# Optimization experiments

Hardware: AMD Instinct MI355X
Metric: run time of the kernel (lower is better)

## Reference

```python
import jax, jax.numpy as jnp
import numpy as np

N_CLUSTERS = 512
FEAT_DIM = 256
ALPHA = 1.0


def setup_inputs() -> dict:
    key = jax.random.key(0)
    kx, kc = jax.random.split(key)
    x = jax.random.normal(kx, (262144, FEAT_DIM), dtype=jnp.float32)
    # xavier_normal for [n_clusters, feat_dim]: std = sqrt(2/(fan_in+fan_out))
    std = float(np.sqrt(2.0 / (N_CLUSTERS + FEAT_DIM)))
    clusters = jax.random.normal(kc, (N_CLUSTERS, FEAT_DIM), dtype=jnp.float32) * std
    return {"x": x, "clusters": clusters}


def reference(x, clusters):
    x_sq = jnp.sum(x * x, axis=1, keepdims=True)            # [N, 1]
    c_sq = jnp.sum(clusters * clusters, axis=1)[None, :]     # [1, K]
    cross = jnp.einsum('nd,kd->nk', x, clusters)             # [N, K]
    dist2 = jnp.maximum(x_sq + c_sq - 2.0 * cross, 0.0) / ALPHA
    q = 1.0 / (1.0 + dist2)
    q = q ** ((ALPHA + 1.0) / 2.0)
    return q / jnp.sum(q, axis=1, keepdims=True)
```

## Files before the change

### kernel.cpp

```cpp
#include <hip/hip_runtime.h>
#include <cstdint>
#include <cstddef>

#define N_ROWS  262144
#define FEAT    256
#define NCLUST  512

#define BM      64
#define THREADS 512

typedef __attribute__((ext_vector_type(8))) __bf16 bf16x8;
typedef __attribute__((ext_vector_type(4))) float  floatx4;

__device__ __forceinline__ unsigned short f2bf(float f) {
    union { float f; unsigned u; } v; v.f = f;
    unsigned u = v.u;
    u += 0x7FFFu + ((u >> 16) & 1u);
    return (unsigned short)(u >> 16);
}

__global__ __launch_bounds__(64) void prep_kernel(const float* __restrict__ clusters,
                                                  unsigned short* __restrict__ cb,
                                                  float* __restrict__ csq) {
    const int row = blockIdx.x;
    const int t   = threadIdx.x;
    const float4* src = (const float4*)(clusters + (size_t)row * FEAT);
    float4 v = src[t];
    float ss = v.x*v.x + v.y*v.y + v.z*v.z + v.w*v.w;
    ushort4 o;
    o.x = f2bf(v.x); o.y = f2bf(v.y); o.z = f2bf(v.z); o.w = f2bf(v.w);

    const int ntile = row >> 4;
    const int l16   = row & 15;
    const int kk    = t >> 3;
    const int quad  = (t >> 1) & 3;
    const int half  = t & 1;
    const size_t g  = (size_t)((ntile * 8 + kk) * 64 + quad * 16 + l16);
    *(ushort4*)(cb + g * 8 + half * 4) = o;

    #pragma unroll
    for (int m = 32; m > 0; m >>= 1) ss += __shfl_xor(ss, m);
    if (t == 0) csq[row] = ss;
}

__global__ __launch_bounds__(THREADS, 4) void cluster_kernel(
    const float* __restrict__ x,
    const unsigned short* __restrict__ cb,
    const float* __restrict__ csq,
    float* __restrict__ out)
{
    __shared__ unsigned short As[BM][FEAT + 8];
    __shared__ float s_xsq[BM];
    __shared__ float s_rpart[8][BM];
    __shared__ float s_rinv[BM];

    const int tid  = threadIdx.x;
    const int row0 = blockIdx.x * BM;

    {
        const int r = tid >> 3;
        const int j = tid & 7;
        const float4* xg = (const float4*)(x + (size_t)(row0 + r) * FEAT);
        float ss = 0.f;
        #pragma unroll
        for (int i = 0; i < 8; i++) {
            float4 v = xg[j + 8 * i];
            ss += v.x*v.x + v.y*v.y + v.z*v.z + v.w*v.w;
            ushort4 o;
            o.x = f2bf(v.x); o.y = f2bf(v.y); o.z = f2bf(v.z); o.w = f2bf(v.w);
            *(ushort4*)&As[r][(j + 8 * i) * 4] = o;
        }
        ss += __shfl_xor(ss, 1);
        ss += __shfl_xor(ss, 2);
        ss += __shfl_xor(ss, 4);
        if (j == 0) s_xsq[r] = ss;
    }
    __syncthreads();

    const int wave = tid >> 6;
    const int lane = tid & 63;
    const int quad = lane >> 4;
    const int l16  = lane & 15;

    floatx4 acc[4][4];
    #pragma unroll
    for (int mt = 0; mt < 4; mt++)
        #pragma unroll
        for (int nt = 0; nt < 4; nt++)
            acc[mt][nt] = (floatx4){0.f, 0.f, 0.f, 0.f};

    const unsigned short* bq[4];
    #pragma unroll
    for (int nt = 0; nt < 4; nt++)
        bq[nt] = cb + ((size_t)((wave * 4 + nt) * 8) * 64 + lane) * 8;

    #pragma unroll 2
    for (int s = 0; s < 8; s++) {
        bf16x8 a[4], b[4];
        #pragma unroll
        for (int mt = 0; mt < 4; mt++)
            a[mt] = *(const bf16x8*)&As[mt * 16 + l16][s * 32 + quad * 8];
        #pragma unroll
        for (int nt = 0; nt < 4; nt++)
            b[nt] = *(const bf16x8*)(bq[nt] + (size_t)s * 512);
        #pragma unroll
        for (int mt = 0; mt < 4; mt++)
            #pragma unroll
            for (int nt = 0; nt < 4; nt++)
                acc[mt][nt] = __builtin_amdgcn_mfma_f32_16x16x32_bf16(
                    a[mt], b[nt], acc[mt][nt], 0, 0, 0);
    }

    float csqv[4];
    #pragma unroll
    for (int nt = 0; nt < 4; nt++)
        csqv[nt] = csq[wave * 64 + nt * 16 + l16];

    #pragma unroll
    for (int mt = 0; mt < 4; mt++) {
        #pragma unroll
        for (int r = 0; r < 4; r++) {
            const int m = mt * 16 + quad * 4 + r;
            float xs = s_xsq[m];
            float rp = 0.f;
            #pragma unroll
            for (int nt = 0; nt < 4; nt++) {
                float d2 = xs + csqv[nt] - 2.0f * acc[mt][nt][r];
                d2 = fmaxf(d2, 0.f);
                float q = __builtin_amdgcn_rcpf(1.0f + d2);
                acc[mt][nt][r] = q;
                rp += q;
            }
            rp += __shfl_xor(rp, 1);
            rp += __shfl_xor(rp, 2);
            rp += __shfl_xor(rp, 4);
            rp += __shfl_xor(rp, 8);
            if (l16 == 0) s_rpart[wave][m] = rp;
        }
    }
    __syncthreads();
    if (tid < BM) {
        float t = 0.f;
        #pragma unroll
        for (int w = 0; w < 8; w++) t += s_rpart[w][tid];
        s_rinv[tid] = __builtin_amdgcn_rcpf(t);
    }
    __syncthreads();

    float* op = out + (size_t)row0 * NCLUST + wave * 64 + l16;
    #pragma unroll
    for (int mt = 0; mt < 4; mt++) {
        #pragma unroll
        for (int r = 0; r < 4; r++) {
            const int m = mt * 16 + quad * 4 + r;
            const float inv = s_rinv[m];
            #pragma unroll
            for (int nt = 0; nt < 4; nt++)
                op[(size_t)m * NCLUST + nt * 16] = acc[mt][nt][r] * inv;
        }
    }
}

extern "C" void kernel_launch(void* const* d_in, const int* in_sizes, int n_in,
                              void* d_out, int out_size, void* d_ws, size_t ws_size,
                              hipStream_t stream) {
    const float* x        = (const float*)d_in[0];
    const float* clusters = (const float*)d_in[1];
    unsigned short* cb = (unsigned short*)d_ws;
    float* csq = (float*)((char*)d_ws + (size_t)NCLUST * FEAT * 2);
    float* out = (float*)d_out;

    prep_kernel<<<NCLUST, 64, 0, stream>>>(clusters, cb, csq);
    cluster_kernel<<<N_ROWS / BM, THREADS, 0, stream>>>(x, cb, csq, out);
}
```

Before: 751.2 us.

## Make cluster kernel persistent with double-buffered prefetch of next x tile

Launches a fixed grid of 512 blocks that each loop over several 64-row tiles, prefetching the next tile's x rows into registers during the MFMA and epilogue of the current tile and writing them into a second LDS buffer. The aim is to hide global load latency of x behind compute and output stores, and to amortize block launch and cluster-norm loads. It doubles LDS use and adds register pressure, which can lower occupancy and reduce the latency hiding that many independent blocks previously gave.

```diff
diff --git a/kernel.cpp b/kernel.cpp
--- a/kernel.cpp
+++ b/kernel.cpp
@@ -8,6 +8,9 @@
 
 #define BM      64
 #define THREADS 512
+#define NTILES  (N_ROWS / BM)
+#define GRID    512
+#define TPB     (NTILES / GRID)
 
 typedef __attribute__((ext_vector_type(8))) __bf16 bf16x8;
 typedef __attribute__((ext_vector_type(4))) float  floatx4;
@@ -49,114 +52,166 @@
     const float* __restrict__ csq,
     float* __restrict__ out)
 {
-    __shared__ unsigned short As[BM][FEAT + 8];
-    __shared__ float s_xsq[BM];
+    __shared__ unsigned short As[2][BM][FEAT + 8];
+    __shared__ float s_xsq[2][BM];
     __shared__ float s_rpart[8][BM];
     __shared__ float s_rinv[BM];
 
     const int tid  = threadIdx.x;
-    const int row0 = blockIdx.x * BM;
-
-    {
-        const int r = tid >> 3;
-        const int j = tid & 7;
-        const float4* xg = (const float4*)(x + (size_t)(row0 + r) * FEAT);
-        float ss = 0.f;
-        #pragma unroll
-        for (int i = 0; i < 8; i++) {
-            float4 v = xg[j + 8 * i];
-            ss += v.x*v.x + v.y*v.y + v.z*v.z + v.w*v.w;
-            ushort4 o;
-            o.x = f2bf(v.x); o.y = f2bf(v.y); o.z = f2bf(v.z); o.w = f2bf(v.w);
-            *(ushort4*)&As[r][(j + 8 * i) * 4] = o;
-        }
-        ss += __shfl_xor(ss, 1);
-        ss += __shfl_xor(ss, 2);
-        ss += __shfl_xor(ss, 4);
-        if (j == 0) s_xsq[r] = ss;
-    }
-    __syncthreads();
+    const int r    = tid >> 3;
+    const int j    = tid & 7;
 
     const int wave = tid >> 6;
     const int lane = tid & 63;
     const int quad = lane >> 4;
     const int l16  = lane & 15;
 
-    floatx4 acc[4][4];
-    #pragma unroll
-    for (int mt = 0; mt < 4; mt++)
-        #pragma unroll
-        for (int nt = 0; nt < 4; nt++)
-            acc[mt][nt] = (floatx4){0.f, 0.f, 0.f, 0.f};
+    const int tile0 = blockIdx.x * TPB;
 
     const unsigned short* bq[4];
     #pragma unroll
     for (int nt = 0; nt < 4; nt++)
         bq[nt] = cb + ((size_t)((wave * 4 + nt) * 8) * 64 + lane) * 8;
 
-    #pragma unroll 2
-    for (int s = 0; s < 8; s++) {
-        bf16x8 a[4], b[4];
-        #pragma unroll
-        for (int mt = 0; mt < 4; mt++)
-            a[mt] = *(const bf16x8*)&As[mt * 16 + l16][s * 32 + quad * 8];
-        #pragma unroll
-        for (int nt = 0; nt < 4; nt++)
-            b[nt] = *(const bf16x8*)(bq[nt] + (size_t)s * 512);
-        #pragma unroll
-        for (int mt = 0; mt < 4; mt++)
-            #pragma unroll
-            for (int nt = 0; nt < 4; nt++)
-                acc[mt][nt] = __builtin_amdgcn_mfma_f32_16x16x32_bf16(
-                    a[mt], b[nt], acc[mt][nt], 0, 0, 0);
-    }
-
     float csqv[4];
     #pragma unroll
     for (int nt = 0; nt < 4; nt++)
         csqv[nt] = csq[wave * 64 + nt * 16 + l16];
 
-    #pragma unroll
-    for (int mt = 0; mt < 4; mt++) {
-        #pragma unroll
-        for (int r = 0; r < 4; r++) {
-            const int m = mt * 16 + quad * 4 + r;
-            float xs = s_xsq[m];
-            float rp = 0.f;
-            #pragma unroll
-            for (int nt = 0; nt < 4; nt++) {
-                float d2 = xs + csqv[nt] - 2.0f * acc[mt][nt][r];
-                d2 = fmaxf(d2, 0.f);
-                float q = __builtin_amdgcn_rcpf(1.0f + d2);
-                acc[mt][nt][r] = q;
-                rp += q;
-            }
-            rp += __shfl_xor(rp, 1);
-            rp += __shfl_xor(rp, 2);
-            rp += __shfl_xor(rp, 4);
-            rp += __shfl_xor(rp, 8);
-            if (l16 == 0) s_rpart[wave][m] = rp;
-        }
+    float4 xa[4], xb[4];
+    {
+        const float4* xg = (const float4*)(x + (size_t)(tile0 * BM + r) * FEAT);
+        #pragma unroll
+        for (int i = 0; i < 4; i++) xa[i] = xg[j + 8 * i];
+        #pragma unroll
+        for (int i = 0; i < 4; i++) xb[i] = xg[j + 8 * i + 32];
+        float ss = 0.f;
+        #pragma unroll
+        for (int i = 0; i < 4; i++) {
+            float4 v = xa[i];
+            ss += v.x*v.x + v.y*v.y + v.z*v.z + v.w*v.w;
+            ushort4 o; o.x = f2bf(v.x); o.y = f2bf(v.y); o.z = f2bf(v.z); o.w = f2bf(v.w);
+            *(ushort4*)&As[0][r][(j + 8 * i) * 4] = o;
+        }
+        #pragma unroll
+        for (int i = 0; i < 4; i++) {
+            float4 v = xb[i];
+            ss += v.x*v.x + v.y*v.y + v.z*v.z + v.w*v.w;
+            ushort4 o; o.x = f2bf(v.x); o.y = f2bf(v.y); o.z = f2bf(v.z); o.w = f2bf(v.w);
+            *(ushort4*)&As[0][r][(j + 8 * i + 32) * 4] = o;
+        }
+        ss += __shfl_xor(ss, 1);
+        ss += __shfl_xor(ss, 2);
+        ss += __shfl_xor(ss, 4);
+        if (j == 0) s_xsq[0][r] = ss;
     }
     __syncthreads();
-    if (tid < BM) {
-        float t = 0.f;
-        #pragma unroll
-        for (int w = 0; w < 8; w++) t += s_rpart[w][tid];
-        s_rinv[tid] = __builtin_amdgcn_rcpf(t);
-    }
-    __syncthreads();
-
-    float* op = out + (size_t)row0 * NCLUST + wave * 64 + l16;
-    #pragma unroll
-    for (int mt = 0; mt < 4; mt++) {
-        #pragma unroll
-        for (int r = 0; r < 4; r++) {
-            const int m = mt * 16 + quad * 4 + r;
-            const float inv = s_rinv[m];
+
+    for (int it = 0; it < TPB; it++) {
+        const int  c       = it & 1;
+        const int  tile    = tile0 + it;
+        const bool hasnext = (it + 1 < TPB);
+        const float4* xg1  = (const float4*)(x + (size_t)((tile + 1) * BM + r) * FEAT);
+
+        if (hasnext) {
+            #pragma unroll
+            for (int i = 0; i < 4; i++) xa[i] = xg1[j + 8 * i];
+        }
+
+        floatx4 acc[4][4];
+        #pragma unroll
+        for (int mt = 0; mt < 4; mt++)
             #pragma unroll
             for (int nt = 0; nt < 4; nt++)
-                op[(size_t)m * NCLUST + nt * 16] = acc[mt][nt][r] * inv;
+                acc[mt][nt] = (floatx4){0.f, 0.f, 0.f, 0.f};
+
+        #pragma unroll 2
+        for (int s = 0; s < 8; s++) {
+            bf16x8 a[4], b[4];
+            #pragma unroll
+            for (int mt = 0; mt < 4; mt++)
+                a[mt] = *(const bf16x8*)&As[c][mt * 16 + l16][s * 32 + quad * 8];
+            #pragma unroll
+            for (int nt = 0; nt < 4; nt++)
+                b[nt] = *(const bf16x8*)(bq[nt] + (size_t)s * 512);
+            #pragma unroll
+            for (int mt = 0; mt < 4; mt++)
+                #pragma unroll
+                for (int nt = 0; nt < 4; nt++)
+                    acc[mt][nt] = __builtin_amdgcn_mfma_f32_16x16x32_bf16(
+                        a[mt], b[nt], acc[mt][nt], 0, 0, 0);
+        }
+
+        if (hasnext) {
+            #pragma unroll
+            for (int i = 0; i < 4; i++) xb[i] = xg1[j + 8 * i + 32];
+        }
+
+        #pragma unroll
+        for (int mt = 0; mt < 4; mt++) {
+            #pragma unroll
+            for (int rr = 0; rr < 4; rr++) {
+                const int m = mt * 16 + quad * 4 + rr;
+                float xs = s_xsq[c][m];
+                float rp = 0.f;
+                #pragma unroll
+                for (int nt = 0; nt < 4; nt++) {
+                    float d2 = xs + csqv[nt] - 2.0f * acc[mt][nt][rr];
+                    d2 = fmaxf(d2, 0.f);
+                    float q = __builtin_amdgcn_rcpf(1.0f + d2);
+                    acc[mt][nt][rr] = q;
+                    rp += q;
+                }
+                rp += __shfl_xor(rp, 1);
+                rp += __shfl_xor(rp, 2);
+                rp += __shfl_xor(rp, 4);
+                rp += __shfl_xor(rp, 8);
+                if (l16 == 0) s_rpart[wave][m] = rp;
+            }
+        }
+        __syncthreads();
+
+        if (tid < BM) {
+            float t = 0.f;
+            #pragma unroll
+            for (int w = 0; w < 8; w++) t += s_rpart[w][tid];
+            s_rinv[tid] = __builtin_amdgcn_rcpf(t);
+        }
+
+        if (hasnext) {
+            float ss = 0.f;
+            #pragma unroll
+            for (int i = 0; i < 4; i++) {
+                float4 v = xa[i];
+                ss += v.x*v.x + v.y*v.y + v.z*v.z + v.w*v.w;
+                ushort4 o; o.x = f2bf(v.x); o.y = f2bf(v.y); o.z = f2bf(v.z); o.w = f2bf(v.w);
+                *(ushort4*)&As[1 - c][r][(j + 8 * i) * 4] = o;
+            }
+            #pragma unroll
+            for (int i = 0; i < 4; i++) {
+                float4 v = xb[i];
+                ss += v.x*v.x + v.y*v.y + v.z*v.z + v.w*v.w;
+                ushort4 o; o.x = f2bf(v.x); o.y = f2bf(v.y); o.z = f2bf(v.z); o.w = f2bf(v.w);
+                *(ushort4*)&As[1 - c][r][(j + 8 * i + 32) * 4] = o;
+            }
+            ss += __shfl_xor(ss, 1);
+            ss += __shfl_xor(ss, 2);
+            ss += __shfl_xor(ss, 4);
+            if (j == 0) s_xsq[1 - c][r] = ss;
+        }
+        __syncthreads();
+
+        float* op = out + (size_t)(tile * BM) * NCLUST + wave * 64 + l16;
+        #pragma unroll
+        for (int mt = 0; mt < 4; mt++) {
+            #pragma unroll
+            for (int rr = 0; rr < 4; rr++) {
+                const int m = mt * 16 + quad * 4 + rr;
+                const float inv = s_rinv[m];
+                #pragma unroll
+                for (int nt = 0; nt < 4; nt++)
+                    op[(size_t)m * NCLUST + nt * 16] = acc[mt][nt][rr] * inv;
+            }
         }
     }
 }
@@ -171,5 +226,5 @@
     float* out = (float*)d_out;
 
     prep_kernel<<<NCLUST, 64, 0, stream>>>(clusters, cb, csq);
-    cluster_kernel<<<N_ROWS / BM, THREADS, 0, stream>>>(x, cb, csq, out);
-}
+    cluster_kernel<<<GRID, THREADS, 0, stream>>>(x, cb, csq, out);
+}
```

After: 866.5 us. 15.4% more time.
